# Performance work log

Measured on AMD Instinct MI355X. Metric: run time of the kernel, lower is better.

Reference implementation:

```python
import jax, jax.numpy as jnp
import numpy as np

DIM = 1024

def setup_inputs() -> dict:
    key = jax.random.key(0)
    k1, k2, k3, k4 = jax.random.split(key, 4)
    x = jax.random.normal(k1, (4, 4096, DIM), dtype=jnp.float32)
    A = jax.random.normal(k2, (DIM, DIM), dtype=jnp.float32) * 0.01
    B_w = jax.random.normal(k3, (DIM, DIM), dtype=jnp.float32) * (1.0 / np.sqrt(DIM))
    C_w = jax.random.normal(k4, (DIM, DIM), dtype=jnp.float32) * (1.0 / np.sqrt(DIM))
    D = jnp.ones((DIM,), dtype=jnp.float32)
    return {"x": x, "A": A, "B_w": B_w, "C_w": C_w, "D": D}

def reference(x, A, B_w, C_w, D):
    # x: [B, L, Dm]; recurrence: h_t = tanh(h_{t-1} @ A.T + x_t @ B_w.T)
    #                 y_t = h_t @ C_w.T + D * x_t
    Bsz, L, Dm = x.shape
    # Precompute the input projection for all steps at once (one big GEMM).
    bx = jnp.einsum('bld,ed->ble', x, B_w)  # [B, L, Dm]

    def step(h, inputs):
        bx_t, x_t = inputs
        h = jnp.tanh(h @ A.T + bx_t)
        y = h @ C_w.T + D * x_t
        return h, y

    h0 = jnp.zeros((Bsz, Dm), dtype=x.dtype)
    # scan over time axis: move L to leading dim
    _, ys = jax.lax.scan(step, h0, (jnp.swapaxes(bx, 0, 1), jnp.swapaxes(x, 0, 1)))
    return jnp.swapaxes(ys, 0, 1)  # [B, L, Dm]
```

## Files before the change

### kernel.cpp

```cpp
#include <hip/hip_runtime.h>
#include <math.h>

#define DM   1024
#define BSZ  4
#define LSEQ 4096
#define GPB  32
#define RPW  32
#define TPB  512
#define SEGC 64
#define SSP  68
#define HSW2 1088
#define CRS  1092

typedef unsigned long long u64;

__global__ __launch_bounds__(256) void bx_gemm_kernel(
    const float* __restrict__ X, const float* __restrict__ Bw,
    float* __restrict__ out)
{
    __shared__ float xs[16][68];
    __shared__ float bs[16][68];
    const int bm = blockIdx.x, bn = blockIdx.y;
    const int t  = threadIdx.x;
    const int tx = t & 15, ty = t >> 4;
    const int ml = t >> 2;
    const int kq = (t & 3) * 4;
    const float* xg = X  + (size_t)(bm * 64 + ml) * DM + kq;
    const float* bg = Bw + (size_t)(bn * 64 + ml) * DM + kq;
    float acc[4][4] = {};
    for (int k0 = 0; k0 < DM; k0 += 16) {
        float4 xv = *(const float4*)(xg + k0);
        float4 bv = *(const float4*)(bg + k0);
        __syncthreads();
        xs[kq+0][ml] = xv.x; xs[kq+1][ml] = xv.y; xs[kq+2][ml] = xv.z; xs[kq+3][ml] = xv.w;
        bs[kq+0][ml] = bv.x; bs[kq+1][ml] = bv.y; bs[kq+2][ml] = bv.z; bs[kq+3][ml] = bv.w;
        __syncthreads();
        #pragma unroll
        for (int kk = 0; kk < 16; ++kk) {
            float a[4], c[4];
            #pragma unroll
            for (int i = 0; i < 4; ++i) a[i] = xs[kk][ty*4+i];
            #pragma unroll
            for (int j = 0; j < 4; ++j) c[j] = bs[kk][tx*4+j];
            #pragma unroll
            for (int i = 0; i < 4; ++i)
                #pragma unroll
                for (int j = 0; j < 4; ++j)
                    acc[i][j] += a[i] * c[j];
        }
    }
    #pragma unroll
    for (int i = 0; i < 4; ++i) {
        float4 v = make_float4(acc[i][0], acc[i][1], acc[i][2], acc[i][3]);
        *(float4*)(out + (size_t)(bm*64 + ty*4 + i)*DM + bn*64 + tx*4) = v;
    }
}

__global__ __launch_bounds__(TPB, 2) void scan_kernel(
    const float* __restrict__ A, const float* __restrict__ Cw,
    const float* __restrict__ Dv, const float* __restrict__ X,
    float* __restrict__ Y, u64* hbuf)
{
    extern __shared__ float lds[];
    float* cs  = lds;
    float* hs0 = lds + RPW * CRS;
    const int b   = blockIdx.x >> 5;
    const int gw  = blockIdx.x & 31;
    const int r0  = gw * RPW;
    const int t   = threadIdx.x;
    const int row = t >> 4;
    const int seg = t & 15;
    const bool lead = (seg == 0);

    float ra[SEGC];
    {
        const float* Ap = A + (size_t)(r0 + row) * DM + seg * SEGC;
        #pragma unroll
        for (int u = 0; u < SEGC / 4; ++u) {
            float4 v = *(const float4*)(Ap + u*4);
            ra[u*4+0]=v.x; ra[u*4+1]=v.y; ra[u*4+2]=v.z; ra[u*4+3]=v.w;
        }
    }
    for (int i = 0; i < 16; ++i) {
        int idx = i * TPB + t;
        int rr  = idx >> 8;
        int c4  = idx & 255;
        float4 v = *(const float4*)(Cw + (size_t)(r0 + rr) * DM + c4 * 4);
        *(float4*)(cs + rr * CRS + (c4 >> 4) * SSP + (c4 & 15) * 4) = v;
    }
    const float dv = Dv[r0 + row];
    __syncthreads();

    const int c0 = t, c1 = t + 512;
    const int s0 = (c0 >> 6) * SSP + (c0 & 63);
    const int s1 = (c1 >> 6) * SSP + (c1 & 63);

    u64 v0 = __hip_atomic_load(hbuf + (size_t)b * DM + c0, __ATOMIC_RELAXED, __HIP_MEMORY_SCOPE_AGENT);
    u64 v1 = __hip_atomic_load(hbuf + (size_t)b * DM + c1, __ATOMIC_RELAXED, __HIP_MEMORY_SCOPE_AGENT);
    float bxv = 0.f;
    float xv  = 0.f;
    if (lead) bxv = Y[(size_t)b*LSEQ*DM + r0 + row];

    for (int k = 0; k <= LSEQ; ++k) {
        const unsigned tag = (unsigned)k;
        u64* src = hbuf + (size_t)(k & 1) * BSZ * DM + (size_t)b * DM;

        int spins = 0;
        while ((((unsigned)(v0 >> 32)) != tag || ((unsigned)(v1 >> 32)) != tag)
               && ++spins < (1 << 20)) {
            if ((unsigned)(v0 >> 32) != tag)
                v0 = __hip_atomic_load(src + c0, __ATOMIC_RELAXED, __HIP_MEMORY_SCOPE_AGENT);
            if ((unsigned)(v1 >> 32) != tag)
                v1 = __hip_atomic_load(src + c1, __ATOMIC_RELAXED, __HIP_MEMORY_SCOPE_AGENT);
        }
        float* hsk = hs0 + (k & 1) * HSW2;
        hsk[s0] = __uint_as_float((unsigned)v0);
        hsk[s1] = __uint_as_float((unsigned)v1);
        __syncthreads();

        const float4* h4p = (const float4*)(hsk + seg * SSP);
        float xv_next = xv;
        if (k < LSEQ) {
            float accA = 0.f;
            #pragma unroll
            for (int u = 0; u < SEGC / 4; ++u) {
                float4 h4 = h4p[u];
                accA += ra[u*4+0]*h4.x + ra[u*4+1]*h4.y + ra[u*4+2]*h4.z + ra[u*4+3]*h4.w;
            }
            accA += __shfl_xor(accA, 1);
            accA += __shfl_xor(accA, 2);
            accA += __shfl_xor(accA, 4);
            accA += __shfl_xor(accA, 8);
            if (lead) {
                float hv = tanhf(accA + bxv);
                u64 pk = ((u64)(unsigned)(k + 1) << 32) | (u64)__float_as_uint(hv);
                __hip_atomic_store(hbuf + (size_t)((k+1) & 1) * BSZ * DM + (size_t)b * DM + r0 + row,
                                   pk, __ATOMIC_RELAXED, __HIP_MEMORY_SCOPE_AGENT);
            }
            u64* srcN = hbuf + (size_t)((k+1) & 1) * BSZ * DM + (size_t)b * DM;
            v0 = __hip_atomic_load(srcN + c0, __ATOMIC_RELAXED, __HIP_MEMORY_SCOPE_AGENT);
            v1 = __hip_atomic_load(srcN + c1, __ATOMIC_RELAXED, __HIP_MEMORY_SCOPE_AGENT);
            if (lead) {
                xv_next = X[(size_t)b*LSEQ*DM + (size_t)k*DM + r0 + row];
                if (k + 1 < LSEQ)
                    bxv = Y[(size_t)b*LSEQ*DM + (size_t)(k+1)*DM + r0 + row];
            }
        }

        if (k > 0) {
            float accC = 0.f;
            const float4* c4p = (const float4*)(cs + row * CRS + seg * SSP);
            #pragma unroll
            for (int u = 0; u < SEGC / 4; ++u) {
                float4 c4 = c4p[u];
                float4 h4 = h4p[u];
                accC += c4.x*h4.x + c4.y*h4.y + c4.z*h4.z + c4.w*h4.w;
            }
            accC += __shfl_xor(accC, 1);
            accC += __shfl_xor(accC, 2);
            accC += __shfl_xor(accC, 4);
            accC += __shfl_xor(accC, 8);
            if (lead) {
                const size_t yoff = (size_t)b*LSEQ*DM + (size_t)(k-1)*DM + r0 + row;
                Y[yoff] = accC + dv * xv;
            }
        }
        xv = xv_next;
    }
}

extern "C" void kernel_launch(void* const* d_in, const int* in_sizes, int n_in,
                              void* d_out, int out_size, void* d_ws, size_t ws_size,
                              hipStream_t stream)
{
    const float* X  = (const float*)d_in[0];
    const float* A  = (const float*)d_in[1];
    const float* Bw = (const float*)d_in[2];
    const float* Cw = (const float*)d_in[3];
    const float* Dv = (const float*)d_in[4];
    float* Y   = (float*)d_out;
    u64* hbuf  = (u64*)d_ws;

    hipMemsetAsync(d_ws, 0, (size_t)2 * BSZ * DM * sizeof(u64), stream);

    dim3 g1((BSZ * LSEQ) / 64, DM / 64);
    bx_gemm_kernel<<<g1, 256, 0, stream>>>(X, Bw, Y);
    const size_t lds_bytes = (size_t)(RPW * CRS + 2 * HSW2) * sizeof(float);
    scan_kernel<<<BSZ * GPB, TPB, lds_bytes, stream>>>(A, Cw, Dv, X, Y, hbuf);
}
```

Baseline: 11.07 ms.

## Place scan blocks per XCD and poll workgroup-scope L2 mirror with agent-scope fallback

Launches 256 blocks and keeps only the ones whose blockIdx mod 8 is below 4. With round-robin dispatch across the eight XCDs, each batch's 32 blocks should then land on one XCD and share its L2. The hidden state is published twice: to a fast buffer with a workgroup-scope store and to a safe buffer with an agent-scope store. Consumers poll the fast buffer with workgroup-scope atomic RMWs, which are meant to resolve in the shared L2, and fall back to agent-scope polling of the safe buffer if the fast path stalls. The aim is to cut cross-step synchronization latency, at the cost of depending on undocumented block-to-XCD placement and extra stores and polling traffic.

```diff
diff --git a/kernel.cpp b/kernel.cpp
--- a/kernel.cpp
+++ b/kernel.cpp
@@ -56,17 +56,44 @@
     }
 }
 
-__global__ __launch_bounds__(TPB, 2) void scan_kernel(
+__device__ __forceinline__ u64 poll_word(u64* fast, u64* safe, unsigned tag,
+                                         u64 v, int& fastok)
+{
+    if ((unsigned)(v >> 32) == tag) return v;
+    if (fastok) {
+        #pragma unroll 1
+        for (int i = 0; i < 16; ++i) {
+            v = __hip_atomic_fetch_add(fast, 0ULL, __ATOMIC_RELAXED,
+                                       __HIP_MEMORY_SCOPE_WORKGROUP);
+            if ((unsigned)(v >> 32) == tag) return v;
+        }
+    }
+    int spins = 0;
+    do {
+        v = __hip_atomic_load(safe, __ATOMIC_RELAXED, __HIP_MEMORY_SCOPE_AGENT);
+    } while ((unsigned)(v >> 32) != tag && ++spins < (1 << 20));
+    if (fastok) {
+        u64 f = __hip_atomic_fetch_add(fast, 0ULL, __ATOMIC_RELAXED,
+                                       __HIP_MEMORY_SCOPE_WORKGROUP);
+        if ((unsigned)(f >> 32) != tag) fastok = 0;
+    }
+    return v;
+}
+
+__global__ __launch_bounds__(TPB, 1) void scan_kernel(
     const float* __restrict__ A, const float* __restrict__ Cw,
     const float* __restrict__ Dv, const float* __restrict__ X,
-    float* __restrict__ Y, u64* hbuf)
-{
+    float* __restrict__ Y, u64* hfast, u64* hsafe)
+{
+    const int r = blockIdx.x & 7;
+    if (r >= BSZ) return;
+    const int b  = r;
+    const int gw = blockIdx.x >> 3;
+    const int r0 = gw * RPW;
+
     extern __shared__ float lds[];
     float* cs  = lds;
     float* hs0 = lds + RPW * CRS;
-    const int b   = blockIdx.x >> 5;
-    const int gw  = blockIdx.x & 31;
-    const int r0  = gw * RPW;
     const int t   = threadIdx.x;
     const int row = t >> 4;
     const int seg = t & 15;
@@ -94,25 +121,23 @@
     const int c0 = t, c1 = t + 512;
     const int s0 = (c0 >> 6) * SSP + (c0 & 63);
     const int s1 = (c1 >> 6) * SSP + (c1 & 63);
-
-    u64 v0 = __hip_atomic_load(hbuf + (size_t)b * DM + c0, __ATOMIC_RELAXED, __HIP_MEMORY_SCOPE_AGENT);
-    u64 v1 = __hip_atomic_load(hbuf + (size_t)b * DM + c1, __ATOMIC_RELAXED, __HIP_MEMORY_SCOPE_AGENT);
+    int fastok = 1;
+
+    u64 v0 = __hip_atomic_load(hsafe + (size_t)b * DM + c0, __ATOMIC_RELAXED, __HIP_MEMORY_SCOPE_AGENT);
+    u64 v1 = __hip_atomic_load(hsafe + (size_t)b * DM + c1, __ATOMIC_RELAXED, __HIP_MEMORY_SCOPE_AGENT);
     float bxv = 0.f;
     float xv  = 0.f;
     if (lead) bxv = Y[(size_t)b*LSEQ*DM + r0 + row];
 
     for (int k = 0; k <= LSEQ; ++k) {
         const unsigned tag = (unsigned)k;
-        u64* src = hbuf + (size_t)(k & 1) * BSZ * DM + (size_t)b * DM;
-
-        int spins = 0;
-        while ((((unsigned)(v0 >> 32)) != tag || ((unsigned)(v1 >> 32)) != tag)
-               && ++spins < (1 << 20)) {
-            if ((unsigned)(v0 >> 32) != tag)
-                v0 = __hip_atomic_load(src + c0, __ATOMIC_RELAXED, __HIP_MEMORY_SCOPE_AGENT);
-            if ((unsigned)(v1 >> 32) != tag)
-                v1 = __hip_atomic_load(src + c1, __ATOMIC_RELAXED, __HIP_MEMORY_SCOPE_AGENT);
-        }
+        const size_t slot = (size_t)(k & 1) * BSZ * DM + (size_t)b * DM;
+        int dummy = 0;
+        int& fo = (k == 0) ? dummy : fastok;
+
+        v0 = poll_word(hfast + slot + c0, hsafe + slot + c0, tag, v0, fo);
+        v1 = poll_word(hfast + slot + c1, hsafe + slot + c1, tag, v1, fo);
+
         float* hsk = hs0 + (k & 1) * HSW2;
         hsk[s0] = __uint_as_float((unsigned)v0);
         hsk[s1] = __uint_as_float((unsigned)v1);
@@ -131,15 +156,24 @@
             accA += __shfl_xor(accA, 2);
             accA += __shfl_xor(accA, 4);
             accA += __shfl_xor(accA, 8);
+            const size_t nslot = (size_t)((k+1) & 1) * BSZ * DM + (size_t)b * DM;
             if (lead) {
                 float hv = tanhf(accA + bxv);
                 u64 pk = ((u64)(unsigned)(k + 1) << 32) | (u64)__float_as_uint(hv);
-                __hip_atomic_store(hbuf + (size_t)((k+1) & 1) * BSZ * DM + (size_t)b * DM + r0 + row,
-                                   pk, __ATOMIC_RELAXED, __HIP_MEMORY_SCOPE_AGENT);
-            }
-            u64* srcN = hbuf + (size_t)((k+1) & 1) * BSZ * DM + (size_t)b * DM;
-            v0 = __hip_atomic_load(srcN + c0, __ATOMIC_RELAXED, __HIP_MEMORY_SCOPE_AGENT);
-            v1 = __hip_atomic_load(srcN + c1, __ATOMIC_RELAXED, __HIP_MEMORY_SCOPE_AGENT);
+                __hip_atomic_store(hfast + nslot + r0 + row, pk,
+                                   __ATOMIC_RELAXED, __HIP_MEMORY_SCOPE_WORKGROUP);
+                __hip_atomic_store(hsafe + nslot + r0 + row, pk,
+                                   __ATOMIC_RELAXED, __HIP_MEMORY_SCOPE_AGENT);
+            }
+            if (fastok) {
+                v0 = __hip_atomic_fetch_add(hfast + nslot + c0, 0ULL,
+                                            __ATOMIC_RELAXED, __HIP_MEMORY_SCOPE_WORKGROUP);
+                v1 = __hip_atomic_fetch_add(hfast + nslot + c1, 0ULL,
+                                            __ATOMIC_RELAXED, __HIP_MEMORY_SCOPE_WORKGROUP);
+            } else {
+                v0 = __hip_atomic_load(hsafe + nslot + c0, __ATOMIC_RELAXED, __HIP_MEMORY_SCOPE_AGENT);
+                v1 = __hip_atomic_load(hsafe + nslot + c1, __ATOMIC_RELAXED, __HIP_MEMORY_SCOPE_AGENT);
+            }
             if (lead) {
                 xv_next = X[(size_t)b*LSEQ*DM + (size_t)k*DM + r0 + row];
                 if (k + 1 < LSEQ)
@@ -178,13 +212,14 @@
     const float* Bw = (const float*)d_in[2];
     const float* Cw = (const float*)d_in[3];
     const float* Dv = (const float*)d_in[4];
-    float* Y   = (float*)d_out;
-    u64* hbuf  = (u64*)d_ws;
-
-    hipMemsetAsync(d_ws, 0, (size_t)2 * BSZ * DM * sizeof(u64), stream);
+    float* Y    = (float*)d_out;
+    u64* hfast  = (u64*)d_ws;
+    u64* hsafe  = hfast + (size_t)2 * BSZ * DM;
+
+    hipMemsetAsync(d_ws, 0, (size_t)4 * BSZ * DM * sizeof(u64), stream);
 
     dim3 g1((BSZ * LSEQ) / 64, DM / 64);
     bx_gemm_kernel<<<g1, 256, 0, stream>>>(X, Bw, Y);
     const size_t lds_bytes = (size_t)(RPW * CRS + 2 * HSW2) * sizeof(float);
-    scan_kernel<<<BSZ * GPB, TPB, lds_bytes, stream>>>(A, Cw, Dv, X, Y, hbuf);
-}
+    scan_kernel<<<256, TPB, lds_bytes, stream>>>(A, Cw, Dv, X, Y, hfast, hsafe);
+}
```

Measured after the change: 10.70 ms. -3.3%, faster.
